# Kernel tuning notes

Measured on AMD Instinct MI355X. Metric: run time of the kernel, lower is better.

## Reference

```python
import jax, jax.numpy as jnp
import numpy as np

WIN = 9  # local window size per spatial dim

def _boxfilter3d(x):
    k = jnp.ones((1, 1, WIN, WIN, WIN), x.dtype) / float(WIN ** 3)
    return jax.lax.conv_general_dilated(
        x, k, window_strides=(1, 1, 1), padding='SAME',
        dimension_numbers=('NCDHW', 'OIDHW', 'NCDHW'))

def setup_inputs() -> dict:
    key = jax.random.key(0)
    k1, k2 = jax.random.split(key)
    shape = (2, 1, 160, 192, 160)
    y_true = jax.random.uniform(k1, shape, dtype=jnp.float32)
    y_pred = jax.random.uniform(k2, shape, dtype=jnp.float32)
    return {"y_true": y_true, "y_pred": y_pred}

def reference(y_true, y_pred):
    Ii, Ji = y_true, y_pred
    mu1 = _boxfilter3d(Ii)
    mu2 = _boxfilter3d(Ji)
    sigma1_sq = _boxfilter3d(Ii * Ii) - mu1 * mu1
    sigma2_sq = _boxfilter3d(Ji * Ji) - mu2 * mu2
    sigma12 = _boxfilter3d(Ii * Ji) - mu1 * mu2
    cc = (sigma12 * sigma12) / (sigma1_sq * sigma2_sq + 1e-5)
    return -jnp.mean(cc)
```

## Files before the change

kernel.cpp:

```cpp
#include <hip/hip_runtime.h>

#define DD 160
#define HH 192
#define WW 160
#define HWs (HH * WW)
#define NTOT 9830400.0f
#define DOUT 20
#define NIT  28
#define NBLK 960

#define SDRS 62
#define SDP  1492
#define HSRS 10
#define HSC  162
#define HSP  810

typedef float    v4 __attribute__((ext_vector_type(4)));
typedef _Float16 h4 __attribute__((ext_vector_type(4)));
typedef _Float16 h2 __attribute__((ext_vector_type(2)));
typedef _Float16 h8 __attribute__((ext_vector_type(8)));

__device__ __forceinline__ void block_sync_lds() {
    __builtin_amdgcn_s_waitcnt(0xc07f);
    __builtin_amdgcn_s_barrier();
}
__device__ __forceinline__ v4 up(h4 x) { return __builtin_convertvector(x, v4); }
__device__ __forceinline__ h4 dnp(v4 x) {
    h2 a = __builtin_bit_cast(h2, __builtin_amdgcn_cvt_pkrtz(x[0], x[1]));
    h2 b = __builtin_bit_cast(h2, __builtin_amdgcn_cvt_pkrtz(x[2], x[3]));
    return __builtin_shufflevector(a, b, 0, 1, 2, 3);
}

__global__ __launch_bounds__(256, 4) void kf(const float* __restrict__ I,
                                             const float* __restrict__ J,
                                             float* __restrict__ partial) {
    __shared__ __align__(16) h4 SDL[2 * SDP];
    __shared__ __align__(16) h4 HSL[2 * HSP];
    __shared__ float red[256];

    const int tid = threadIdx.x;
    const int wgid = blockIdx.x;
    const int tl = (wgid & 7) * 120 + (wgid >> 3);
    const int bx = tl % 60, by = (tl / 60) % 8, b = tl / 480;
    const int w0 = (bx % 5) * 32, h0 = (bx / 5) * 16;
    const int d0 = by * DOUT;
    const int bid = tl;

    const int rt = tid ^ ((bx & 1) << 7);

    const bool p1 = rt < 240;
    const int r = rt / 10, g = rt % 10;
    const int gh = h0 - 4 + r, gw = w0 - 4 + g * 4;
    const bool colOK = p1 && gh >= 0 && gh < HH && gw >= 0 && gw < WW;
    const size_t colOff = (size_t)gh * WW + gw;
    const float* Ib = I + (size_t)b * DD * HWs + colOff;
    const float* Jb = J + (size_t)b * DD * HWs + colOff;
    const int sdwOff = r * SDRS + (r >> 3) * 2 + 6 * g;

    const bool p2 = rt < 100;
    const int g2 = rt % 10, ch2 = (rt / 10) % 5, hh0 = (rt / 50) * 8;
    const int sdrOff = hh0 * SDRS + (hh0 >> 3) * 2 + 6 * g2 +
                       (ch2 == 4 ? 4 + (g2 & 1) : ch2);
    const int hswOff = ch2 * HSC + hh0 * HSRS + g2;

    const bool p3 = rt >= 128;
    const int q3 = rt & 127;
    const int hh = q3 >> 3, sg = q3 & 7;
    const int hsrOff = hh * HSRS + sg;

    v4 sd0 = 0.f, sd1 = 0.f, sd2 = 0.f, sd3 = 0.f, sd4 = 0.f;
    v4 pLI = 0.f, pLJ = 0.f;
    v4 pOI = 0.f, pOJ = 0.f;
    float acc = 0.f;
    const float inv = 1.0f / 729.0f;

    {
        const int si = d0 - 4;
        if (colOK && si >= 0) {
            pLI = *(const v4*)(Ib + (size_t)si * HWs);
            pLJ = *(const v4*)(Jb + (size_t)si * HWs);
        }
    }

#pragma unroll
    for (int t = 0; t < NIT + 2; ++t) {
        if (t < NIT && p1) {
            const v4 cI = pLI, cJ = pLJ;
            v4 dI = cI, dJv = cJ;
            v4 dII = cI * cI, dJJ = cJ * cJ, dIJ = cI * cJ;
            if (t >= 9) {
                dI  -= pOI;        dJv -= pOJ;
                dII -= pOI * pOI;  dJJ -= pOJ * pOJ;  dIJ -= pOI * pOJ;
            }
            sd0 += dI; sd1 += dJv; sd2 += dII; sd3 += dJJ; sd4 += dIJ;
            h4* const qb = &SDL[(t & 1) * SDP + sdwOff];
            h4 c0 = dnp(sd0), c1 = dnp(sd1), c2 = dnp(sd2), c3 = dnp(sd3);
            *(h8*)qb       = __builtin_shufflevector(c0, c1, 0,1,2,3,4,5,6,7);
            *(h8*)(qb + 2) = __builtin_shufflevector(c2, c3, 0,1,2,3,4,5,6,7);
            qb[4 + (g & 1)] = dnp(sd4);
            pLI = 0.f; pLJ = 0.f;
            const int sn = d0 - 3 + t;
            if (t + 1 < NIT && colOK && sn >= 0 && sn < DD) {
                pLI = *(const v4*)(Ib + (size_t)sn * HWs);
                pLJ = *(const v4*)(Jb + (size_t)sn * HWs);
            }
            pOI = 0.f; pOJ = 0.f;
            const int so = d0 - 12 + t;
            if (t >= 8 && t + 1 < NIT && colOK && so >= 0) {
                pOI = *(const v4*)(Ib + (size_t)so * HWs);
                pOJ = *(const v4*)(Jb + (size_t)so * HWs);
            }
        }

        if (t >= 1 && t <= NIT && p2) {
            const int par = (t - 1) & 1;
            const h4* const sdr = &SDL[par * SDP + sdrOff];
            h4* const hsw = &HSL[par * HSP + hswOff];
            h4 keep[7];
            h4 s = sdr[0];
            keep[0] = s;
#pragma unroll
            for (int k = 1; k < 9; ++k) {
                h4 v = sdr[k * SDRS + (k >= 8 ? 2 : 0)];
                if (k < 7) keep[k] = v;
                s += v;
            }
            hsw[0] = s;
#pragma unroll
            for (int j = 1; j < 8; ++j) {
                s += sdr[(j + 8) * SDRS + 2] - keep[j - 1];
                hsw[j * HSRS] = s;
            }
        }

        if (t >= 10 && p3) {
            const h4* const hsr = &HSL[(t & 1) * HSP + hsrOff];
            float w[5][4];
#pragma unroll
            for (int c = 0; c < 5; ++c) {
                v4 fa = up(hsr[c * HSC]);
                v4 fb = up(hsr[c * HSC + 1]);
                v4 fc = up(hsr[c * HSC + 2]);
                float s = fa[0] + fa[1] + fa[2] + fa[3] +
                          fb[0] + fb[1] + fb[2] + fb[3] + fc[0];
                w[c][0] = s;
                s += fc[1] - fa[0]; w[c][1] = s;
                s += fc[2] - fa[1]; w[c][2] = s;
                s += fc[3] - fa[2]; w[c][3] = s;
            }
#pragma unroll
            for (int e = 0; e < 4; ++e) {
                float mu1 = w[0][e] * inv, mu2 = w[1][e] * inv;
                float g1  = fmaf(-mu1, mu1, w[2][e] * inv);
                float g2v = fmaf(-mu2, mu2, w[3][e] * inv);
                float g12 = fmaf(-mu1, mu2, w[4][e] * inv);
                acc += __fdividef(g12 * g12, fmaf(g1, g2v, 1e-5f));
            }
        }

        block_sync_lds();
    }

    red[tid] = acc;
    __syncthreads();
    if (tid < 128) red[tid] += red[tid + 128];
    __syncthreads();
    if (tid < 64) {
        float a = red[tid] + red[tid + 64];
#pragma unroll
        for (int off = 32; off > 0; off >>= 1) a += __shfl_down(a, off);
        if (tid == 0) partial[bid] = a;
    }
}

__global__ void k3_final(const float* __restrict__ partial,
                         float* __restrict__ out) {
    __shared__ float r[1024];
    const int i = threadIdx.x;
    r[i] = (i < NBLK) ? partial[i] : 0.f;
    __syncthreads();
    for (int off = 512; off > 0; off >>= 1) {
        if (i < off) r[i] += r[i + off];
        __syncthreads();
    }
    if (i == 0) out[0] = -r[0] * (1.0f / NTOT);
}

extern "C" void kernel_launch(void* const* d_in, const int* in_sizes, int n_in,
                              void* d_out, int out_size, void* d_ws, size_t ws_size,
                              hipStream_t stream) {
    (void)in_sizes; (void)n_in; (void)out_size; (void)ws_size;
    const float* I = (const float*)d_in[0];
    const float* J = (const float*)d_in[1];
    float* out     = (float*)d_out;
    float* partial = (float*)d_ws;

    kf<<<dim3(NBLK), 256, 0, stream>>>(I, J, partial);
    k3_final<<<1, 1024, 0, stream>>>(partial, out);
}
```

Measured before the change: 141.5 us.

## Process two depth slices per barrier with four-deep LDS ring and two-ahead prefetch

The depth loop is restructured so that each barrier interval handles two slices per stage. It uses four-slot LDS buffers for the depth and H partial sums, and prefetches global loads two slices ahead. This roughly halves the number of block barriers and gives memory loads more latency cover. In exchange, LDS use doubles and launch bounds drop to 2 blocks per SIMD, which may lower occupancy and raise register pressure.

After: 164.3 us. 16.1% more time.

```diff
diff --git a/kernel.cpp b/kernel.cpp
--- a/kernel.cpp
+++ b/kernel.cpp
@@ -31,11 +31,11 @@
     return __builtin_shufflevector(a, b, 0, 1, 2, 3);
 }
 
-__global__ __launch_bounds__(256, 4) void kf(const float* __restrict__ I,
+__global__ __launch_bounds__(256, 2) void kf(const float* __restrict__ I,
                                              const float* __restrict__ J,
                                              float* __restrict__ partial) {
-    __shared__ __align__(16) h4 SDL[2 * SDP];
-    __shared__ __align__(16) h4 HSL[2 * HSP];
+    __shared__ __align__(16) h4 SDL[4 * SDP];
+    __shared__ __align__(16) h4 HSL[4 * HSP];
     __shared__ float red[256];
 
     const int tid = threadIdx.x;
@@ -69,95 +69,104 @@
     const int hsrOff = hh * HSRS + sg;
 
     v4 sd0 = 0.f, sd1 = 0.f, sd2 = 0.f, sd3 = 0.f, sd4 = 0.f;
-    v4 pLI = 0.f, pLJ = 0.f;
-    v4 pOI = 0.f, pOJ = 0.f;
+    v4 pLI0 = 0.f, pLJ0 = 0.f, pLI1 = 0.f, pLJ1 = 0.f;
+    v4 pOI0 = 0.f, pOJ0 = 0.f, pOI1 = 0.f, pOJ1 = 0.f;
     float acc = 0.f;
     const float inv = 1.0f / 729.0f;
 
     {
-        const int si = d0 - 4;
-        if (colOK && si >= 0) {
-            pLI = *(const v4*)(Ib + (size_t)si * HWs);
-            pLJ = *(const v4*)(Jb + (size_t)si * HWs);
-        }
-    }
-
-#pragma unroll
-    for (int t = 0; t < NIT + 2; ++t) {
-        if (t < NIT && p1) {
-            const v4 cI = pLI, cJ = pLJ;
-            v4 dI = cI, dJv = cJ;
-            v4 dII = cI * cI, dJJ = cJ * cJ, dIJ = cI * cJ;
-            if (t >= 9) {
-                dI  -= pOI;        dJv -= pOJ;
-                dII -= pOI * pOI;  dJJ -= pOJ * pOJ;  dIJ -= pOI * pOJ;
-            }
-            sd0 += dI; sd1 += dJv; sd2 += dII; sd3 += dJJ; sd4 += dIJ;
-            h4* const qb = &SDL[(t & 1) * SDP + sdwOff];
-            h4 c0 = dnp(sd0), c1 = dnp(sd1), c2 = dnp(sd2), c3 = dnp(sd3);
-            *(h8*)qb       = __builtin_shufflevector(c0, c1, 0,1,2,3,4,5,6,7);
-            *(h8*)(qb + 2) = __builtin_shufflevector(c2, c3, 0,1,2,3,4,5,6,7);
-            qb[4 + (g & 1)] = dnp(sd4);
-            pLI = 0.f; pLJ = 0.f;
-            const int sn = d0 - 3 + t;
-            if (t + 1 < NIT && colOK && sn >= 0 && sn < DD) {
-                pLI = *(const v4*)(Ib + (size_t)sn * HWs);
-                pLJ = *(const v4*)(Jb + (size_t)sn * HWs);
-            }
-            pOI = 0.f; pOJ = 0.f;
-            const int so = d0 - 12 + t;
-            if (t >= 8 && t + 1 < NIT && colOK && so >= 0) {
-                pOI = *(const v4*)(Ib + (size_t)so * HWs);
-                pOJ = *(const v4*)(Jb + (size_t)so * HWs);
-            }
-        }
-
-        if (t >= 1 && t <= NIT && p2) {
-            const int par = (t - 1) & 1;
-            const h4* const sdr = &SDL[par * SDP + sdrOff];
-            h4* const hsw = &HSL[par * HSP + hswOff];
-            h4 keep[7];
-            h4 s = sdr[0];
-            keep[0] = s;
-#pragma unroll
-            for (int k = 1; k < 9; ++k) {
-                h4 v = sdr[k * SDRS + (k >= 8 ? 2 : 0)];
-                if (k < 7) keep[k] = v;
-                s += v;
-            }
-            hsw[0] = s;
-#pragma unroll
-            for (int j = 1; j < 8; ++j) {
-                s += sdr[(j + 8) * SDRS + 2] - keep[j - 1];
-                hsw[j * HSRS] = s;
-            }
-        }
-
-        if (t >= 10 && p3) {
-            const h4* const hsr = &HSL[(t & 1) * HSP + hsrOff];
-            float w[5][4];
-#pragma unroll
-            for (int c = 0; c < 5; ++c) {
-                v4 fa = up(hsr[c * HSC]);
-                v4 fb = up(hsr[c * HSC + 1]);
-                v4 fc = up(hsr[c * HSC + 2]);
-                float s = fa[0] + fa[1] + fa[2] + fa[3] +
-                          fb[0] + fb[1] + fb[2] + fb[3] + fc[0];
-                w[c][0] = s;
-                s += fc[1] - fa[0]; w[c][1] = s;
-                s += fc[2] - fa[1]; w[c][2] = s;
-                s += fc[3] - fa[2]; w[c][3] = s;
-            }
-#pragma unroll
-            for (int e = 0; e < 4; ++e) {
-                float mu1 = w[0][e] * inv, mu2 = w[1][e] * inv;
-                float g1  = fmaf(-mu1, mu1, w[2][e] * inv);
-                float g2v = fmaf(-mu2, mu2, w[3][e] * inv);
-                float g12 = fmaf(-mu1, mu2, w[4][e] * inv);
-                acc += __fdividef(g12 * g12, fmaf(g1, g2v, 1e-5f));
-            }
-        }
-
+        const int s0 = d0 - 4;
+        if (colOK && s0 >= 0) {
+            pLI0 = *(const v4*)(Ib + (size_t)s0 * HWs);
+            pLJ0 = *(const v4*)(Jb + (size_t)s0 * HWs);
+        }
+        const int s1 = d0 - 3;
+        if (colOK && s1 >= 0) {
+            pLI1 = *(const v4*)(Ib + (size_t)s1 * HWs);
+            pLJ1 = *(const v4*)(Jb + (size_t)s1 * HWs);
+        }
+    }
+
+    auto PH1 = [&](int t, v4& pLIs, v4& pLJs, v4& pOIs, v4& pOJs) {
+        const v4 cI = pLIs, cJ = pLJs;
+        v4 dI = cI, dJv = cJ;
+        v4 dII = cI * cI, dJJ = cJ * cJ, dIJ = cI * cJ;
+        if (t >= 9) {
+            dI  -= pOIs;        dJv -= pOJs;
+            dII -= pOIs * pOIs; dJJ -= pOJs * pOJs; dIJ -= pOIs * pOJs;
+        }
+        sd0 += dI; sd1 += dJv; sd2 += dII; sd3 += dJJ; sd4 += dIJ;
+        h4* const qb = &SDL[(t & 3) * SDP + sdwOff];
+        h4 c0 = dnp(sd0), c1 = dnp(sd1), c2 = dnp(sd2), c3 = dnp(sd3);
+        *(h8*)qb       = __builtin_shufflevector(c0, c1, 0,1,2,3,4,5,6,7);
+        *(h8*)(qb + 2) = __builtin_shufflevector(c2, c3, 0,1,2,3,4,5,6,7);
+        qb[4 + (g & 1)] = dnp(sd4);
+        pLIs = 0.f; pLJs = 0.f;
+        const int sn = d0 - 2 + t;
+        if (t + 2 < NIT && colOK && sn >= 0 && sn < DD) {
+            pLIs = *(const v4*)(Ib + (size_t)sn * HWs);
+            pLJs = *(const v4*)(Jb + (size_t)sn * HWs);
+        }
+        pOIs = 0.f; pOJs = 0.f;
+        const int so = d0 - 11 + t;
+        if (t + 2 >= 9 && t + 2 < NIT && colOK && so >= 0) {
+            pOIs = *(const v4*)(Ib + (size_t)so * HWs);
+            pOJs = *(const v4*)(Jb + (size_t)so * HWs);
+        }
+    };
+
+    auto PH2 = [&](int s) {
+        const h4* const sdr = &SDL[(s & 3) * SDP + sdrOff];
+        h4* const hsw = &HSL[(s & 3) * HSP + hswOff];
+        h4 keep[7];
+        h4 sum = sdr[0];
+        keep[0] = sum;
+#pragma unroll
+        for (int kk = 1; kk < 9; ++kk) {
+            h4 v = sdr[kk * SDRS + (kk >= 8 ? 2 : 0)];
+            if (kk < 7) keep[kk] = v;
+            sum += v;
+        }
+        hsw[0] = sum;
+#pragma unroll
+        for (int j = 1; j < 8; ++j) {
+            sum += sdr[(j + 8) * SDRS + 2] - keep[j - 1];
+            hsw[j * HSRS] = sum;
+        }
+    };
+
+    auto PH3 = [&](int s) {
+        const h4* const hsr = &HSL[(s & 3) * HSP + hsrOff];
+        float w[5][4];
+#pragma unroll
+        for (int c = 0; c < 5; ++c) {
+            v4 fa = up(hsr[c * HSC]);
+            v4 fb = up(hsr[c * HSC + 1]);
+            v4 fc = up(hsr[c * HSC + 2]);
+            float s0 = fa[0] + fa[1] + fa[2] + fa[3] +
+                       fb[0] + fb[1] + fb[2] + fb[3] + fc[0];
+            w[c][0] = s0;
+            s0 += fc[1] - fa[0]; w[c][1] = s0;
+            s0 += fc[2] - fa[1]; w[c][2] = s0;
+            s0 += fc[3] - fa[2]; w[c][3] = s0;
+        }
+#pragma unroll
+        for (int e = 0; e < 4; ++e) {
+            float mu1 = w[0][e] * inv, mu2 = w[1][e] * inv;
+            float g1  = fmaf(-mu1, mu1, w[2][e] * inv);
+            float g2v = fmaf(-mu2, mu2, w[3][e] * inv);
+            float g12 = fmaf(-mu1, mu2, w[4][e] * inv);
+            acc += __fdividef(g12 * g12, fmaf(g1, g2v, 1e-5f));
+        }
+    };
+
+#pragma unroll
+    for (int k = 0; k < 16; ++k) {
+        const int t0 = 2 * k, t1 = 2 * k + 1;
+        if (t0 < NIT && p1) PH1(t0, pLI0, pLJ0, pOI0, pOJ0);
+        if (t1 < NIT && p1) PH1(t1, pLI1, pLJ1, pOI1, pOJ1);
+        if (k >= 1 && k <= 14 && p2) { PH2(2 * k - 2); PH2(2 * k - 1); }
+        if (k >= 6 && p3)            { PH3(2 * k - 4); PH3(2 * k - 3); }
         block_sync_lds();
     }
 
```
